# Kernel tuning notes

Hardware: AMD Instinct MI355X
Metric: run time of the kernel (lower is better)

Reference implementation:

```python
import jax, jax.numpy as jnp
import numpy as np
from jax import lax

OBS_LEN = 8
PRED_LEN = 12
DIM = 128      # hidden_dim
EMB = 64       # embedding_dim
HEADS = 4
MODES = 5
SCENE = 32     # peds per scene
NPED = 8192    # total peds (256 scenes)


def _lin(key, out_d, in_d):
    kw, kb = jax.random.split(key)
    w = jax.random.normal(kw, (out_d, in_d), jnp.float32) / np.sqrt(in_d).astype(np.float32)
    b = jax.random.normal(kb, (out_d,), jnp.float32) * 0.01
    return w, b


def _stack(key, n, out_d, in_d):
    ws, bs = zip(*[_lin(k, out_d, in_d) for k in jax.random.split(key, n)])
    return jnp.stack(ws), jnp.stack(bs)


def setup_inputs() -> dict:
    key = jax.random.key(0)
    ks = jax.random.split(key, 24)
    inp = {}
    inp['obs_traj'] = jax.random.normal(ks[0], (OBS_LEN, NPED, 2), jnp.float32)
    inp['pe_w'], inp['pe_b'] = _lin(ks[1], EMB, 2)
    inp['lstm_wih'], inp['lstm_bih'] = _lin(ks[2], 4 * DIM, EMB)
    inp['lstm_whh'], inp['lstm_bhh'] = _lin(ks[3], 4 * DIM, DIM)
    inp['rp_w1'], inp['rp_b1'] = _lin(ks[4], DIM // 2, 2)
    inp['rp_w2'], inp['rp_b2'] = _lin(ks[5], DIM, DIM // 2)
    inp['wq'], inp['bq'] = _lin(ks[6], DIM, DIM)
    inp['wk'], inp['bk'] = _lin(ks[7], DIM, DIM)
    inp['wv'], inp['bv'] = _lin(ks[8], DIM, DIM)
    inp['wo'], inp['bo'] = _lin(ks[9], DIM, DIM)
    inp['op_w'], inp['op_b'] = _lin(ks[10], DIM, 2 * DIM)
    inp['mp_w1'], inp['mp_b1'] = _lin(ks[11], DIM, 2 * DIM)
    inp['mp_w2'], inp['mp_b2'] = _lin(ks[12], MODES, DIM)
    inp['td_w1'], inp['td_b1'] = _stack(ks[13], MODES, DIM, 2 * DIM)
    inp['td_w2'], inp['td_b2'] = _stack(ks[14], MODES, DIM, DIM)
    inp['td_w3'], inp['td_b3'] = _stack(ks[15], MODES, PRED_LEN * 2, DIM)
    inp['ud_w1'], inp['ud_b1'] = _stack(ks[16], MODES, DIM // 2, 2 * DIM)
    inp['ud_w2'], inp['ud_b2'] = _stack(ks[17], MODES, PRED_LEN * 2, DIM // 2)
    inp['scene_size'] = SCENE
    return inp


def reference(obs_traj, pe_w, pe_b, lstm_wih, lstm_bih, lstm_whh, lstm_bhh,
              rp_w1, rp_b1, rp_w2, rp_b2, wq, bq, wk, bk, wv, bv, wo, bo,
              op_w, op_b, mp_w1, mp_b1, mp_w2, mp_b2,
              td_w1, td_b1, td_w2, td_b2, td_w3, td_b3,
              ud_w1, ud_b1, ud_w2, ud_b2, scene_size):
    obs = jnp.transpose(obs_traj, (1, 0, 2))          # (N, T, 2)
    N = obs.shape[0]
    D = lstm_whh.shape[1]

    # ---- NodeHistoryEncoder: Linear embed + 1-layer LSTM, last hidden ----
    emb = jnp.einsum('ntd,ed->nte', obs, pe_w) + pe_b  # (N, T, EMB)

    def step(carry, x):
        h, c = carry
        g = x @ lstm_wih.T + lstm_bih + h @ lstm_whh.T + lstm_bhh
        i, f, gg, o = jnp.split(g, 4, axis=-1)          # torch gate order i,f,g,o
        c = jax.nn.sigmoid(f) * c + jax.nn.sigmoid(i) * jnp.tanh(gg)
        h = jax.nn.sigmoid(o) * jnp.tanh(c)
        return (h, c), None

    h0 = jnp.zeros((N, D), obs.dtype)
    (node_features, _), _ = lax.scan(step, (h0, h0), jnp.swapaxes(emb, 0, 1))
    last_pos = obs[:, -1, :]                            # (N, 2)

    # ---- EdgeEncoder: per-scene rel-pos-biased multi-head attention ----
    S = scene_size
    B = N // S
    feat = node_features.reshape(B, S, D)
    pos = last_pos.reshape(B, S, 2)
    rel = pos[:, None, :, :] - pos[:, :, None, :]       # [b,i,j] = pos_j - pos_i
    rel_enc = jax.nn.relu(jnp.einsum('bijd,hd->bijh', rel, rp_w1) + rp_b1)
    rel_enc = jnp.einsum('bijh,eh->bije', rel_enc, rp_w2) + rp_b2  # (B,S,S,D)
    kv = feat[:, None, :, :] + rel_enc                  # key == value
    dh = D // HEADS
    q = (feat @ wq.T + bq).reshape(B, S, HEADS, dh)
    kp = (jnp.einsum('bijd,ed->bije', kv, wk) + bk).reshape(B, S, S, HEADS, dh)
    vp = (jnp.einsum('bijd,ed->bije', kv, wv) + bv).reshape(B, S, S, HEADS, dh)
    scores = jnp.einsum('bihd,bijhd->bhij', q, kp) / np.sqrt(dh).astype(np.float32)
    attn = jax.nn.softmax(scores, axis=-1)
    ctx = jnp.einsum('bhij,bijhd->bihd', attn, vp).reshape(B, S, D)
    attn_out = ctx @ wo.T + bo
    edge = (jnp.concatenate([feat, attn_out], axis=-1) @ op_w.T + op_b).reshape(N, D)

    f_all = jnp.concatenate([node_features, edge], axis=-1)  # (N, 2D)

    # ---- GMMDecoder ----
    probs = jax.nn.softmax(jax.nn.relu(f_all @ mp_w1.T + mp_b1) @ mp_w2.T + mp_b2, axis=-1)
    h1 = jax.nn.relu(jnp.einsum('nd,mhd->nmh', f_all, td_w1) + td_b1)    # (N,M,D)
    h2 = jax.nn.relu(jnp.einsum('nmh,mgh->nmg', h1, td_w2) + td_b2)
    traj = (jnp.einsum('nmg,mog->nmo', h2, td_w3) + td_b3).reshape(N, MODES, PRED_LEN, 2)
    u1 = jax.nn.relu(jnp.einsum('nd,mhd->nmh', f_all, ud_w1) + ud_b1)
    sigmas = jax.nn.softplus(jnp.einsum('nmh,moh->nmo', u1, ud_w2) + ud_b2).reshape(N, MODES, PRED_LEN, 2)
    predictions = jnp.cumsum(traj, axis=2) + last_pos[:, None, None, :]
    return predictions, probs
```

## Files before the change

### kernel.cpp

```cpp
#include <hip/hip_runtime.h>
#include <math.h>

typedef __attribute__((ext_vector_type(8))) short short8;
typedef __attribute__((ext_vector_type(4))) float f32x4;

#define NPED 8192
#define INVS 0.1767766952966369f

#define B_WHH    0
#define B_WQKV   131072
#define B_WK2PAD 294912
#define B_OPWE   360448
#define B_MPW1   425984
#define B_TDW1   491520
#define B_TDW2   819200
#define B_TDW3C  983040
#define F_WIHE   1024000
#define F_BEFF   1028096
#define F_WV2T   1030144
#define F_BQKV   1062912
#define F_BEDGE  1065472
#define F_TDB3C  1065984
#define A_FEAT   1066496
#define A_QKV    3163648

__device__ __forceinline__ float bf2f(ushort u) {
  union { unsigned i; float f; } v; v.i = ((unsigned)u) << 16; return v.f;
}
__device__ __forceinline__ float blo(unsigned u) {
  union { unsigned i; float f; } v; v.i = u << 16; return v.f;
}
__device__ __forceinline__ float bhi(unsigned u) {
  union { unsigned i; float f; } v; v.i = u & 0xffff0000u; return v.f;
}
__device__ __forceinline__ ushort f2bf(float f) {
  union { float f; unsigned i; } v; v.f = f;
  unsigned r = v.i + 0x7fffu + ((v.i >> 16) & 1u);
  return (ushort)(r >> 16);
}

__global__ __launch_bounds__(256) void prep(
    const float* __restrict__ wih, const float* __restrict__ bih, const float* __restrict__ bhh,
    const float* __restrict__ pew, const float* __restrict__ peb,
    const float* __restrict__ wk, const float* __restrict__ wv,
    const float* __restrict__ rpw2, const float* __restrict__ rpb2,
    const float* __restrict__ bq, const float* __restrict__ bk, const float* __restrict__ bv,
    const float* __restrict__ whh, const float* __restrict__ wq, const float* __restrict__ wo,
    const float* __restrict__ opw, const float* __restrict__ opb, const float* __restrict__ bo,
    const float* __restrict__ mpw1,
    const float* __restrict__ tdw1, const float* __restrict__ tdw2,
    const float* __restrict__ tdw3, const float* __restrict__ tdb3,
    char* __restrict__ wsb) {
  int tid = blockIdx.x * 256 + threadIdx.x;
  if (tid < 512) {
    int d = tid;
    float s0 = 0.f, s1 = 0.f, sb = 0.f;
    for (int e = 0; e < 64; ++e) {
      float w = wih[d * 64 + e];
      s0 += w * pew[e * 2]; s1 += w * pew[e * 2 + 1]; sb += w * peb[e];
    }
    ((float*)(wsb + F_WIHE))[d * 2] = s0;
    ((float*)(wsb + F_WIHE))[d * 2 + 1] = s1;
    ((float*)(wsb + F_BEFF))[d] = bih[d] + bhh[d] + sb;
  } else if (tid < 49664) {
    int j = tid - 512; int n = j >> 7, k = j & 127;
    float v = (n < 128) ? wq[n * 128 + k] * INVS
                        : (n < 256) ? wk[(n - 128) * 128 + k] : wv[(n - 256) * 128 + k];
    ((ushort*)(wsb + B_WQKV))[j] = f2bf(v);
  } else if (tid < 82432) {
    int idx = tid - 49664; int r = idx >> 7, d = idx & 127;
    int h = r >> 6, e = r & 63;
    float s = 0.f;
    if ((d >> 5) == h)
      for (int c = 0; c < 128; ++c) s += wk[d * 128 + c] * rpw2[c * 64 + e];
    ((ushort*)(wsb + B_WK2PAD))[idx] = f2bf(s);
  } else if (tid < 115200) {
    int idx = tid - 82432; int o = idx >> 8, k = idx & 255;
    float s;
    if (k < 128) s = opw[o * 256 + k];
    else {
      s = 0.f;
      for (int c = 0; c < 128; ++c) s += opw[o * 256 + 128 + c] * wo[c * 128 + (k - 128)];
    }
    ((ushort*)(wsb + B_OPWE))[idx] = f2bf(s);
  } else if (tid < 147968) {
    int j = tid - 115200; ((ushort*)(wsb + B_MPW1))[j] = f2bf(mpw1[j]);
  } else if (tid < 311808) {
    int j = tid - 147968; ((ushort*)(wsb + B_TDW1))[j] = f2bf(tdw1[j]);
  } else if (tid < 393728) {
    int j = tid - 311808; ((ushort*)(wsb + B_TDW2))[j] = f2bf(tdw2[j]);
  } else if (tid < 414208) {
    int j = tid - 393728; int m = j >> 12, r = j & 4095, o = r >> 7, k = r & 127;
    float s = 0.f;
    if (o < 24) {
      int c = o & 1, jj = o >> 1;
      for (int jp = 0; jp <= jj; ++jp) s += tdw3[(m * 24 + jp * 2 + c) * 128 + k];
    }
    ((ushort*)(wsb + B_TDW3C))[j] = f2bf(s);
  } else if (tid < 414328) {
    int j = tid - 414208; int m = j / 24, o = j % 24;
    int c = o & 1, jj = o >> 1;
    float s = 0.f;
    for (int jp = 0; jp <= jj; ++jp) s += tdb3[m * 24 + jp * 2 + c];
    ((float*)(wsb + F_TDB3C))[j] = s;
  } else if (tid < 414968) {
    int d = tid - 414328;
    float s = 0.f;
    if (d < 128) s = bq[d] * INVS;
    else if (d < 256) {
      int dd = d - 128; s = bk[dd];
      for (int c = 0; c < 128; ++c) s += wk[dd * 128 + c] * rpb2[c];
    } else if (d < 384) {
      int dd = d - 256; s = bv[dd];
      for (int c = 0; c < 128; ++c) s += wv[dd * 128 + c] * rpb2[c];
    }
    ((float*)(wsb + F_BQKV))[d] = s;
  } else if (tid < 415096) {
    int o = tid - 414968;
    float s = opb[o];
    for (int c = 0; c < 128; ++c) s += opw[o * 256 + 128 + c] * bo[c];
    ((float*)(wsb + F_BEDGE))[o] = s;
  } else if (tid < 423288) {
    int idx = tid - 415096; int e = idx >> 7, hd = idx & 127;
    float s = 0.f;
    for (int c = 0; c < 128; ++c) s += wv[hd * 128 + c] * rpw2[c * 64 + e];
    ((float*)(wsb + F_WV2T))[idx] = s;
  } else if (tid < 488824) {
    int i = tid - 423288;
    ((ushort*)(wsb + B_WHH))[i] = f2bf(whh[i]);
  }
}

__global__ __launch_bounds__(256) void prep2(
    const ushort* __restrict__ wk2pad, const float* __restrict__ wq,
    const float* __restrict__ bq, ushort* __restrict__ wqkv, float* __restrict__ bqkv) {
  int idx = blockIdx.x * 256 + threadIdx.x;
  if (idx < 32768) {
    int e = idx >> 7, k = idx & 127, h = e >> 6;
    float s = 0.f;
    for (int dd = 0; dd < 32; ++dd) {
      int d = h * 32 + dd;
      s += bf2f(wk2pad[e * 128 + d]) * wq[d * 128 + k];
    }
    wqkv[(384 + e) * 128 + k] = f2bf(s * INVS);
  } else if (idx < 33024) {
    int e = idx - 32768, h = e >> 6;
    float s = 0.f;
    for (int dd = 0; dd < 32; ++dd) {
      int d = h * 32 + dd;
      s += bf2f(wk2pad[e * 128 + d]) * bq[d];
    }
    bqkv[384 + e] = s * INVS;
  }
}

__global__ __launch_bounds__(512) void lstm_mfma(
    const float* __restrict__ obs, const ushort* __restrict__ whhb,
    const float* __restrict__ wihe, const float* __restrict__ beff,
    ushort* __restrict__ feat) {
  __shared__ ushort Hs[32 * 128];
  __shared__ float obs_s[8][32][2];
  int tid = threadIdx.x;
  int w = tid >> 6, l = tid & 63;
  int lm = l & 15, lg = l >> 4;
  int nb = blockIdx.x * 32;
  {
    int ts = tid >> 6, p = (tid >> 1) & 31, c = tid & 1;
    obs_s[ts][p][c] = obs[ts * (NPED * 2) + (nb + p) * 2 + c];
  }
  for (int i = tid; i < 4096; i += 512) Hs[i] = 0;
  short8 bfr[4][4];
  float wx0[4], wx1[4], be[4];
#pragma unroll
  for (int q = 0; q < 4; ++q) {
    int g = q * 128 + w * 16 + lm;
    wx0[q] = wihe[g * 2]; wx1[q] = wihe[g * 2 + 1]; be[q] = beff[g];
#pragma unroll
    for (int ks = 0; ks < 4; ++ks)
      bfr[q][ks] = *(const short8*)(const void*)&whhb[g * 128 + ks * 32 + lg * 8];
  }
  float cst[2][4] = {};
  __syncthreads();
  for (int ts = 0; ts < 8; ++ts) {
    f32x4 acc[2][4];
#pragma unroll
    for (int mi = 0; mi < 2; ++mi)
#pragma unroll
      for (int r = 0; r < 4; ++r) {
        int p = mi * 16 + lg * 4 + r;
        float ox = obs_s[ts][p][0], oy = obs_s[ts][p][1];
#pragma unroll
        for (int q = 0; q < 4; ++q)
          acc[mi][q][r] = be[q] + wx0[q] * ox + wx1[q] * oy;
      }
#pragma unroll
    for (int ks = 0; ks < 4; ++ks) {
      int p0 = lm, p1 = 16 + lm;
      short8 a0 = *(const short8*)(const void*)&Hs[p0 * 128 + ((ks * 32 + lg * 8) ^ ((p0 & 7) << 3))];
      short8 a1 = *(const short8*)(const void*)&Hs[p1 * 128 + ((ks * 32 + lg * 8) ^ ((p1 & 7) << 3))];
#pragma unroll
      for (int q = 0; q < 4; ++q) {
        acc[0][q] = __builtin_amdgcn_mfma_f32_16x16x32_bf16(a0, bfr[q][ks], acc[0][q], 0, 0, 0);
        acc[1][q] = __builtin_amdgcn_mfma_f32_16x16x32_bf16(a1, bfr[q][ks], acc[1][q], 0, 0, 0);
      }
    }
    __syncthreads();
    int d = w * 16 + lm;
#pragma unroll
    for (int mi = 0; mi < 2; ++mi)
#pragma unroll
      for (int r = 0; r < 4; ++r) {
        int p = mi * 16 + lg * 4 + r;
        float xi = acc[mi][0][r], xf = acc[mi][1][r], xg = acc[mi][2][r], xo = acc[mi][3][r];
        float ig = 1.f / (1.f + __expf(-xi));
        float fg = 1.f / (1.f + __expf(-xf));
        xg = fminf(fmaxf(xg, -30.f), 30.f);
        float eg = __expf(-2.f * xg);
        float gg = (1.f - eg) / (1.f + eg);
        float og = 1.f / (1.f + __expf(-xo));
        float cv = fg * cst[mi][r] + ig * gg;
        cst[mi][r] = cv;
        float cvc = fminf(fmaxf(cv, -30.f), 30.f);
        float ec = __expf(-2.f * cvc);
        float th = (1.f - ec) / (1.f + ec);
        ushort hb = f2bf(og * th);
        Hs[p * 128 + (d ^ ((p & 7) << 3))] = hb;
        if (ts == 7) feat[(size_t)(nb + p) * 128 + d] = hb;
      }
    __syncthreads();
  }
}

template<int NF, int NKS, int K1KS, int RS>
__global__ __launch_bounds__(256) void mfma_gemm(
    const ushort* __restrict__ A1, int lda1,
    const ushort* __restrict__ A2, int lda2,
    const ushort* __restrict__ Bw,
    const float* __restrict__ bias,
    ushort* __restrict__ out, int ldo, int ooff, int relu) {
  int w = threadIdx.x >> 6, l = threadIdx.x & 63;
  int lm = l & 15, lg = l >> 4;
  int row, col0, orow0;
  if (RS) {
    row = blockIdx.x * 32 + (w >> 1) * 16 + lm;
    col0 = blockIdx.y * (NF * 32) + (w & 1) * (NF * 16);
    orow0 = blockIdx.x * 32 + (w >> 1) * 16 + lg * 4;
  } else {
    row = blockIdx.x * 64 + w * 16 + lm;
    col0 = blockIdx.y * (NF * 16);
    orow0 = blockIdx.x * 64 + w * 16 + lg * 4;
  }
  f32x4 acc[NF];
#pragma unroll
  for (int i = 0; i < NF; ++i) acc[i] = (f32x4){0.f, 0.f, 0.f, 0.f};
#pragma unroll
  for (int ks = 0; ks < NKS; ++ks) {
    int kb = ks * 32 + lg * 8;
    const ushort* ap = (ks < K1KS) ? (A1 + (size_t)row * lda1 + kb)
                                   : (A2 + (size_t)row * lda2 + (kb - K1KS * 32));
    short8 af = *(const short8*)(const void*)ap;
#pragma unroll
    for (int ni = 0; ni < NF; ++ni) {
      short8 bf = *(const short8*)(const void*)(Bw + (size_t)(col0 + ni * 16 + lm) * (NKS * 32) + kb);
      acc[ni] = __builtin_amdgcn_mfma_f32_16x16x32_bf16(af, bf, acc[ni], 0, 0, 0);
    }
  }
#pragma unroll
  for (int ni = 0; ni < NF; ++ni) {
    int c = col0 + ni * 16 + lm;
    float bv = bias[c];
#pragma unroll
    for (int r = 0; r < 4; ++r) {
      float v = acc[ni][r] + bv;
      if (relu) v = fmaxf(v, 0.f);
      out[(size_t)(orow0 + r) * ldo + ooff + c] = f2bf(v);
    }
  }
}

__global__ __launch_bounds__(256) void td_mp(
    const ushort* __restrict__ feat, const ushort* __restrict__ qkv,
    const ushort* __restrict__ w1b, const float* __restrict__ tdb1,
    const ushort* __restrict__ w2b, const float* __restrict__ tdb2,
    const ushort* __restrict__ w3c, const float* __restrict__ b3c,
    const float* __restrict__ mpw1b, const float* __restrict__ mpb1,
    const float* __restrict__ mpw2, const float* __restrict__ mpb2,
    const float* __restrict__ obs, float* __restrict__ out) {
  __shared__ float smem[32 * 72];
  int t = threadIdx.x, w = t >> 6, l = t & 63, lm = l & 15, lg = l >> 4;
  int wr = w >> 1, wc = w & 1;
  int z = blockIdx.y;

  if (z < 5) {
    ushort* slab = (ushort*)smem;
    int m = z;
    int row = blockIdx.x * 32 + wr * 16 + lm;
    const ushort* W1 = w1b + (size_t)m * 32768;
    const ushort* W2 = w2b + (size_t)m * 16384;
    const ushort* W3 = w3c + (size_t)m * 4096;
    const float* B1 = tdb1 + m * 128;
    const float* B2 = tdb2 + m * 128;
    f32x4 a1[4];
#pragma unroll
    for (int i = 0; i < 4; ++i) a1[i] = (f32x4){0.f, 0.f, 0.f, 0.f};
#pragma unroll
    for (int ks = 0; ks < 8; ++ks) {
      int kb = ks * 32 + lg * 8;
      const ushort* ap = (ks < 4) ? (feat + (size_t)row * 128 + kb)
                                  : (qkv + (size_t)row * 640 + 256 + (kb - 128));
      short8 af = *(const short8*)(const void*)ap;
#pragma unroll
      for (int ni = 0; ni < 4; ++ni) {
        short8 bf = *(const short8*)(const void*)(W1 + (size_t)(wc * 64 + ni * 16 + lm) * 256 + kb);
        a1[ni] = __builtin_amdgcn_mfma_f32_16x16x32_bf16(af, bf, a1[ni], 0, 0, 0);
      }
    }
#pragma unroll
    for (int ni = 0; ni < 4; ++ni) {
      int c = wc * 64 + ni * 16 + lm;
      float bb = B1[c];
#pragma unroll
      for (int r = 0; r < 4; ++r)
        slab[(wr * 16 + lg * 4 + r) * 136 + c] = f2bf(fmaxf(a1[ni][r] + bb, 0.f));
    }
    __syncthreads();
    short8 af2[4];
#pragma unroll
    for (int ks = 0; ks < 4; ++ks)
      af2[ks] = *(const short8*)(const void*)&slab[(wr * 16 + lm) * 136 + ks * 32 + lg * 8];
    f32x4 a2[4];
#pragma unroll
    for (int i = 0; i < 4; ++i) a2[i] = (f32x4){0.f, 0.f, 0.f, 0.f};
#pragma unroll
    for (int ks = 0; ks < 4; ++ks) {
      int kb = ks * 32 + lg * 8;
#pragma unroll
      for (int ni = 0; ni < 4; ++ni) {
        short8 bf = *(const short8*)(const void*)(W2 + (size_t)(wc * 64 + ni * 16 + lm) * 128 + kb);
        a2[ni] = __builtin_amdgcn_mfma_f32_16x16x32_bf16(af2[ks], bf, a2[ni], 0, 0, 0);
      }
    }
    __syncthreads();
#pragma unroll
    for (int ni = 0; ni < 4; ++ni) {
      int c = wc * 64 + ni * 16 + lm;
      float bb = B2[c];
#pragma unroll
      for (int r = 0; r < 4; ++r)
        slab[(wr * 16 + lg * 4 + r) * 136 + c] = f2bf(fmaxf(a2[ni][r] + bb, 0.f));
    }
    __syncthreads();
    short8 af3[4], w3f[4];
#pragma unroll
    for (int ks = 0; ks < 4; ++ks) {
      af3[ks] = *(const short8*)(const void*)&slab[(wr * 16 + lm) * 136 + ks * 32 + lg * 8];
      w3f[ks] = *(const short8*)(const void*)(W3 + (size_t)(wc * 16 + lm) * 128 + ks * 32 + lg * 8);
    }
    f32x4 a3 = (f32x4){0.f, 0.f, 0.f, 0.f};
#pragma unroll
    for (int ks = 0; ks < 4; ++ks)
      a3 = __builtin_amdgcn_mfma_f32_16x16x32_bf16(af3[ks], w3f[ks], a3, 0, 0, 0);
    int o = wc * 16 + lm;
    if (o < 24) {
      float bb = b3c[m * 24 + o];
      int c = o & 1;
#pragma unroll
      for (int r = 0; r < 4; ++r) {
        int n = blockIdx.x * 32 + wr * 16 + lg * 4 + r;
        out[(size_t)n * 120 + m * 24 + o] = a3[r] + bb + obs[7 * (NPED * 2) + n * 2 + c];
      }
    }
  } else {
    float* w2s = smem;
    float* pc  = smem + 640;
    for (int i = t; i < 640; i += 256) w2s[(i >> 7) * 128 + (i & 127)] = mpw2[i];
    int g = wr, ch = wc, cb = ch * 64;
    int row = blockIdx.x * 32 + g * 16 + lm;
    f32x4 acc[4];
#pragma unroll
    for (int i = 0; i < 4; ++i) acc[i] = (f32x4){0.f, 0.f, 0.f, 0.f};
#pragma unroll
    for (int ks = 0; ks < 8; ++ks) {
      int kb = ks * 32 + lg * 8;
      const ushort* ap = (ks < 4) ? (feat + (size_t)row * 128 + kb)
                                  : (qkv + (size_t)row * 640 + 256 + (kb - 128));
      short8 af = *(const short8*)(const void*)ap;
#pragma unroll
      for (int ni = 0; ni < 4; ++ni) {
        short8 bf = *(const short8*)(const void*)((const ushort*)mpw1b + (size_t)(cb + ni * 16 + lm) * 256 + kb);
        acc[ni] = __builtin_amdgcn_mfma_f32_16x16x32_bf16(af, bf, acc[ni], 0, 0, 0);
      }
    }
    __syncthreads();
    float bc[4];
#pragma unroll
    for (int ni = 0; ni < 4; ++ni) bc[ni] = mpb1[cb + ni * 16 + lm];
    float lgt[4][5];
#pragma unroll
    for (int r = 0; r < 4; ++r)
#pragma unroll
      for (int m = 0; m < 5; ++m) {
        float s = 0.f;
#pragma unroll
        for (int ni = 0; ni < 4; ++ni)
          s += fmaxf(acc[ni][r] + bc[ni], 0.f) * w2s[m * 128 + cb + ni * 16 + lm];
        lgt[r][m] = s;
      }
#pragma unroll
    for (int mask = 1; mask < 16; mask <<= 1)
#pragma unroll
      for (int r = 0; r < 4; ++r)
#pragma unroll
        for (int m = 0; m < 5; ++m)
          lgt[r][m] += __shfl_xor(lgt[r][m], mask);
    if (ch == 1 && lm < 5) {
#pragma unroll
      for (int r = 0; r < 4; ++r) pc[(g * 16 + lg * 4 + r) * 5 + lm] = lgt[r][lm];
    }
    __syncthreads();
    if (ch == 0 && lm < 5) {
#pragma unroll
      for (int r = 0; r < 4; ++r) {
        float lv[5], mx = -1e30f, sm = 0.f;
#pragma unroll
        for (int m = 0; m < 5; ++m) {
          lv[m] = lgt[r][m] + pc[(g * 16 + lg * 4 + r) * 5 + m] + mpb2[m];
          mx = fmaxf(mx, lv[m]);
        }
#pragma unroll
        for (int m = 0; m < 5; ++m) { lv[m] = expf(lv[m] - mx); sm += lv[m]; }
        int n = blockIdx.x * 32 + g * 16 + lg * 4 + r;
        out[983040 + (size_t)n * 5 + lm] = lv[lm] / sm;
      }
    }
  }
}

__global__ __launch_bounds__(256) void attn_kernel(
    const float* __restrict__ obs, ushort* QKV,
    const float* __restrict__ wv2T,
    const float* __restrict__ rpw1, const float* __restrict__ rpb1) {
  __shared__ ushort K0s[32 * 128];
  __shared__ ushort V0s[32 * 128];
  __shared__ ushort renc[4 * 32 * 64];
  __shared__ float Qi[4][128];
  __shared__ float QWs[4][256];
  __shared__ float att[4][4][32];
  __shared__ float AR[4][4][64];
  __shared__ float rpx[64], rpy[64], rpb[64];
  __shared__ float posS[32][2];
  __shared__ float posI[4][2];
  int t = threadIdx.x;
  int scene = blockIdx.x & 255, ic = blockIdx.x >> 8;
  int i0 = ic * 4, sbase = scene * 32;

  for (int idx = t; idx < 1024; idx += 256) {
    int arr = idx >> 9, j = (idx >> 4) & 31, c = idx & 15;
    short8 v = *(const short8*)(const void*)&QKV[(size_t)(sbase + j) * 640 + 128 + arr * 128 + c * 8];
    ushort* dst = arr ? V0s : K0s;
    *(short8*)(void*)&dst[j * 128 + (c ^ (j & 7)) * 8] = v;
  }
  for (int idx = t; idx < 512; idx += 256) {
    int ii = idx >> 7, d = idx & 127;
    Qi[ii][d] = bf2f(QKV[(size_t)(sbase + i0 + ii) * 640 + d]);
  }
  for (int idx = t; idx < 1024; idx += 256) {
    int ii = idx >> 8, e = idx & 255;
    QWs[ii][e] = bf2f(QKV[(size_t)(sbase + i0 + ii) * 640 + 384 + e]);
  }
  if (t < 64) posS[t >> 1][t & 1] = obs[7 * (NPED * 2) + (sbase + (t >> 1)) * 2 + (t & 1)];
  else if (t < 72) {
    int q = t - 64;
    posI[q >> 1][q & 1] = obs[7 * (NPED * 2) + (sbase + i0 + (q >> 1)) * 2 + (q & 1)];
  } else if (t >= 128 && t < 192) {
    int e = t - 128;
    rpx[e] = rpw1[e * 2]; rpy[e] = rpw1[e * 2 + 1]; rpb[e] = rpb1[e];
  }
  __syncthreads();

  for (int idx = t; idx < 1024; idx += 256) {
    int ii = idx >> 8, j = (idx >> 3) & 31, c = idx & 7;
    float dx = posS[j][0] - posI[ii][0], dy = posS[j][1] - posI[ii][1];
    short8 pk;
#pragma unroll
    for (int r = 0; r < 8; ++r) {
      int e = c * 8 + r;
      pk[r] = (short)f2bf(fmaxf(rpx[e] * dx + rpy[e] * dy + rpb[e], 0.f));
    }
    *(short8*)(void*)&renc[(ii * 32 + j) * 64 + (c ^ (j & 7)) * 8] = pk;
  }
  __syncthreads();

  for (int idx = t; idx < 512; idx += 256) {
    int ii = idx >> 7, h = (idx >> 5) & 3, j = idx & 31;
    float s = 0.f;
#pragma unroll
    for (int cc = 0; cc < 4; ++cc) {
      uint4 kv = *(const uint4*)(const void*)&K0s[j * 128 + (((h * 4 + cc) ^ (j & 7)) * 8)];
      const float4 qa = *(const float4*)&Qi[ii][h * 32 + cc * 8];
      const float4 qb = *(const float4*)&Qi[ii][h * 32 + cc * 8 + 4];
      s += blo(kv.x) * qa.x + bhi(kv.x) * qa.y + blo(kv.y) * qa.z + bhi(kv.y) * qa.w;
      s += blo(kv.z) * qb.x + bhi(kv.z) * qb.y + blo(kv.w) * qb.z + bhi(kv.w) * qb.w;
    }
#pragma unroll
    for (int c = 0; c < 8; ++c) {
      uint4 rv = *(const uint4*)(const void*)&renc[(ii * 32 + j) * 64 + ((c ^ (j & 7)) * 8)];
      const float4 ua = *(const float4*)&QWs[ii][h * 64 + c * 8];
      const float4 ub = *(const float4*)&QWs[ii][h * 64 + c * 8 + 4];
      s += blo(rv.x) * ua.x + bhi(rv.x) * ua.y + blo(rv.y) * ua.z + bhi(rv.y) * ua.w;
      s += blo(rv.z) * ub.x + bhi(rv.z) * ub.y + blo(rv.w) * ub.z + bhi(rv.w) * ub.w;
    }
    att[ii][h][j] = s;
  }
  __syncthreads();

  {
    int r = t >> 4, lj = t & 15;
    float v0 = att[r >> 2][r & 3][lj], v1 = att[r >> 2][r & 3][lj + 16];
    float mx = fmaxf(v0, v1);
    mx = fmaxf(mx, __shfl_xor(mx, 8, 16));
    mx = fmaxf(mx, __shfl_xor(mx, 4, 16));
    mx = fmaxf(mx, __shfl_xor(mx, 2, 16));
    mx = fmaxf(mx, __shfl_xor(mx, 1, 16));
    float e0 = expf(v0 - mx), e1 = expf(v1 - mx);
    float sm = e0 + e1;
    sm += __shfl_xor(sm, 8, 16);
    sm += __shfl_xor(sm, 4, 16);
    sm += __shfl_xor(sm, 2, 16);
    sm += __shfl_xor(sm, 1, 16);
    float inv = 1.f / sm;
    att[r >> 2][r & 3][lj] = e0 * inv;
    att[r >> 2][r & 3][lj + 16] = e1 * inv;
  }
  __syncthreads();

  {
    int ii = t >> 6, h = (t >> 4) & 3, e4 = t & 15;
    int c = e4 >> 1, off = (e4 & 1) * 4;
    float a0 = 0.f, a1 = 0.f, a2 = 0.f, a3 = 0.f;
    for (int j = 0; j < 32; ++j) {
      float av = att[ii][h][j];
      uint2 rv = *(const uint2*)(const void*)&renc[(ii * 32 + j) * 64 + ((c ^ (j & 7)) * 8) + off];
      a0 += av * blo(rv.x); a1 += av * bhi(rv.x);
      a2 += av * blo(rv.y); a3 += av * bhi(rv.y);
    }
    *(float4*)&AR[ii][h][e4 * 4] = make_float4(a0, a1, a2, a3);
  }
  __syncthreads();

  {
    int ii = t >> 6, l = t & 63;
    int h5 = l >> 5, hd4 = l & 31;
    int hd = hd4 * 4, h = hd >> 5;
    float c0 = 0.f, c1 = 0.f, c2 = 0.f, c3 = 0.f;
    int cch = hd >> 3, offh = hd & 7;
    for (int j = h5 * 16; j < h5 * 16 + 16; ++j) {
      float av = att[ii][h][j];
      uint2 vv = *(const uint2*)(const void*)&V0s[j * 128 + ((cch ^ (j & 7)) * 8) + offh];
      c0 += av * blo(vv.x); c1 += av * bhi(vv.x);
      c2 += av * blo(vv.y); c3 += av * bhi(vv.y);
    }
    for (int e4 = h5 * 8; e4 < h5 * 8 + 8; ++e4) {
      const float4 ar = *(const float4*)&AR[ii][h][e4 * 4];
#pragma unroll
      for (int r = 0; r < 4; ++r) {
        const float4 wv = *(const float4*)&wv2T[(e4 * 4 + r) * 128 + hd];
        float a = (r == 0) ? ar.x : (r == 1) ? ar.y : (r == 2) ? ar.z : ar.w;
        c0 += a * wv.x; c1 += a * wv.y; c2 += a * wv.z; c3 += a * wv.w;
      }
    }
    c0 += __shfl_xor(c0, 32); c1 += __shfl_xor(c1, 32);
    c2 += __shfl_xor(c2, 32); c3 += __shfl_xor(c3, 32);
    if (h5 == 0) {
      ushort4 o;
      o.x = f2bf(c0); o.y = f2bf(c1); o.z = f2bf(c2); o.w = f2bf(c3);
      *(ushort4*)(void*)&QKV[(size_t)(sbase + i0 + ii) * 640 + hd] = o;
    }
  }
}

extern "C" void kernel_launch(void* const* d_in, const int* in_sizes, int n_in,
                              void* d_out, int out_size, void* d_ws, size_t ws_size,
                              hipStream_t stream) {
  (void)in_sizes; (void)n_in; (void)out_size; (void)ws_size;
  const float* obs  = (const float*)d_in[0];
  const float* pew  = (const float*)d_in[1];
  const float* peb  = (const float*)d_in[2];
  const float* wih  = (const float*)d_in[3];
  const float* bih  = (const float*)d_in[4];
  const float* whh  = (const float*)d_in[5];
  const float* bhh  = (const float*)d_in[6];
  const float* rpw1 = (const float*)d_in[7];
  const float* rpb1 = (const float*)d_in[8];
  const float* rpw2 = (const float*)d_in[9];
  const float* rpb2 = (const float*)d_in[10];
  const float* wq   = (const float*)d_in[11];
  const float* bq   = (const float*)d_in[12];
  const float* wk   = (const float*)d_in[13];
  const float* bk   = (const float*)d_in[14];
  const float* wv   = (const float*)d_in[15];
  const float* bv   = (const float*)d_in[16];
  const float* wo   = (const float*)d_in[17];
  const float* bo   = (const float*)d_in[18];
  const float* opw  = (const float*)d_in[19];
  const float* opb  = (const float*)d_in[20];
  const float* mpw1 = (const float*)d_in[21];
  const float* mpb1 = (const float*)d_in[22];
  const float* mpw2 = (const float*)d_in[23];
  const float* mpb2 = (const float*)d_in[24];
  const float* tdw1 = (const float*)d_in[25];
  const float* tdb1 = (const float*)d_in[26];
  const float* tdw2 = (const float*)d_in[27];
  const float* tdb2 = (const float*)d_in[28];
  const float* tdw3 = (const float*)d_in[29];
  const float* tdb3 = (const float*)d_in[30];
  char* wsb = (char*)d_ws;
  float* out = (float*)d_out;

  ushort* whhb   = (ushort*)(wsb + B_WHH);
  ushort* wqkvb  = (ushort*)(wsb + B_WQKV);
  ushort* wk2pb  = (ushort*)(wsb + B_WK2PAD);
  ushort* opweb  = (ushort*)(wsb + B_OPWE);
  ushort* mpw1b  = (ushort*)(wsb + B_MPW1);
  ushort* tdw1b  = (ushort*)(wsb + B_TDW1);
  ushort* tdw2b  = (ushort*)(wsb + B_TDW2);
  ushort* tdw3cb = (ushort*)(wsb + B_TDW3C);
  ushort* featb  = (ushort*)(wsb + A_FEAT);
  ushort* qkvb   = (ushort*)(wsb + A_QKV);

  prep<<<1910, 256, 0, stream>>>(wih, bih, bhh, pew, peb, wk, wv, rpw2, rpb2,
                                 bq, bk, bv, whh, wq, wo, opw, opb, bo, mpw1,
                                 tdw1, tdw2, tdw3, tdb3, wsb);
  prep2<<<129, 256, 0, stream>>>(wk2pb, wq, bq, wqkvb, (float*)(wsb + F_BQKV));
  lstm_mfma<<<256, 512, 0, stream>>>(obs, whhb, (float*)(wsb + F_WIHE),
                                     (float*)(wsb + F_BEFF), featb);
  mfma_gemm<4, 4, 4, 0><<<dim3(128, 10), 256, 0, stream>>>(
      featb, 128, featb, 128, wqkvb, (float*)(wsb + F_BQKV), qkvb, 640, 0, 0);
  attn_kernel<<<2048, 256, 0, stream>>>(obs, qkvb, (float*)(wsb + F_WV2T), rpw1, rpb1);
  mfma_gemm<2, 8, 4, 1><<<dim3(256, 2), 256, 0, stream>>>(
      featb, 128, qkvb, 640, opweb, (float*)(wsb + F_BEDGE), qkvb, 640, 256, 0);
  td_mp<<<dim3(256, 6), 256, 0, stream>>>(featb, qkvb, tdw1b, tdb1, tdw2b, tdb2,
                                          tdw3cb, (float*)(wsb + F_TDB3C),
                                          (const float*)mpw1b, mpb1, mpw2, mpb2, obs, out);
}
```

Before: 265.5 us.

## Fuse QKV GEMM into LSTM, edge GEMM into decoder, merge prep kernels

The QKV projection now runs at the tail of the LSTM kernel, reading the final hidden state straight from shared memory. The edge projection is recomputed inside each decoder block (six times per row tile) and kept in shared memory. prep2 is folded into prep by recomputing the wk·rpw2 product inline. This removes three kernel launches and the global round trips for feat-to-qkv and edge. In exchange it adds redundant edge GEMM work per z-slice and a heavier serial inner loop in prep.

```diff
diff --git a/kernel.cpp b/kernel.cpp
--- a/kernel.cpp
+++ b/kernel.cpp
@@ -9,20 +9,19 @@
 
 #define B_WHH    0
 #define B_WQKV   131072
-#define B_WK2PAD 294912
-#define B_OPWE   360448
-#define B_MPW1   425984
-#define B_TDW1   491520
-#define B_TDW2   819200
-#define B_TDW3C  983040
-#define F_WIHE   1024000
-#define F_BEFF   1028096
-#define F_WV2T   1030144
-#define F_BQKV   1062912
-#define F_BEDGE  1065472
-#define F_TDB3C  1065984
-#define A_FEAT   1066496
-#define A_QKV    3163648
+#define B_OPWE   294912
+#define B_MPW1   360448
+#define B_TDW1   425984
+#define B_TDW2   753664
+#define B_TDW3C  917504
+#define F_WIHE   958464
+#define F_BEFF   962560
+#define F_WV2T   964608
+#define F_BQKV   997376
+#define F_BEDGE  999936
+#define F_TDB3C  1000448
+#define A_FEAT   1001472
+#define A_QKV    3098624
 
 __device__ __forceinline__ float bf2f(ushort u) {
   union { unsigned i; float f; } v; v.i = ((unsigned)u) << 16; return v.f;
@@ -68,14 +67,7 @@
                         : (n < 256) ? wk[(n - 128) * 128 + k] : wv[(n - 256) * 128 + k];
     ((ushort*)(wsb + B_WQKV))[j] = f2bf(v);
   } else if (tid < 82432) {
-    int idx = tid - 49664; int r = idx >> 7, d = idx & 127;
-    int h = r >> 6, e = r & 63;
-    float s = 0.f;
-    if ((d >> 5) == h)
-      for (int c = 0; c < 128; ++c) s += wk[d * 128 + c] * rpw2[c * 64 + e];
-    ((ushort*)(wsb + B_WK2PAD))[idx] = f2bf(s);
-  } else if (tid < 115200) {
-    int idx = tid - 82432; int o = idx >> 8, k = idx & 255;
+    int idx = tid - 49664; int o = idx >> 8, k = idx & 255;
     float s;
     if (k < 128) s = opw[o * 256 + k];
     else {
@@ -83,81 +75,80 @@
       for (int c = 0; c < 128; ++c) s += opw[o * 256 + 128 + c] * wo[c * 128 + (k - 128)];
     }
     ((ushort*)(wsb + B_OPWE))[idx] = f2bf(s);
-  } else if (tid < 147968) {
-    int j = tid - 115200; ((ushort*)(wsb + B_MPW1))[j] = f2bf(mpw1[j]);
-  } else if (tid < 311808) {
-    int j = tid - 147968; ((ushort*)(wsb + B_TDW1))[j] = f2bf(tdw1[j]);
-  } else if (tid < 393728) {
-    int j = tid - 311808; ((ushort*)(wsb + B_TDW2))[j] = f2bf(tdw2[j]);
-  } else if (tid < 414208) {
-    int j = tid - 393728; int m = j >> 12, r = j & 4095, o = r >> 7, k = r & 127;
+  } else if (tid < 115200) {
+    int j = tid - 82432; ((ushort*)(wsb + B_MPW1))[j] = f2bf(mpw1[j]);
+  } else if (tid < 279040) {
+    int j = tid - 115200; ((ushort*)(wsb + B_TDW1))[j] = f2bf(tdw1[j]);
+  } else if (tid < 360960) {
+    int j = tid - 279040; ((ushort*)(wsb + B_TDW2))[j] = f2bf(tdw2[j]);
+  } else if (tid < 381440) {
+    int j = tid - 360960; int m = j >> 12, r = j & 4095, o = r >> 7, k = r & 127;
     float s = 0.f;
     if (o < 24) {
       int c = o & 1, jj = o >> 1;
       for (int jp = 0; jp <= jj; ++jp) s += tdw3[(m * 24 + jp * 2 + c) * 128 + k];
     }
     ((ushort*)(wsb + B_TDW3C))[j] = f2bf(s);
-  } else if (tid < 414328) {
-    int j = tid - 414208; int m = j / 24, o = j % 24;
+  } else if (tid < 381560) {
+    int j = tid - 381440; int m = j / 24, o = j % 24;
     int c = o & 1, jj = o >> 1;
     float s = 0.f;
     for (int jp = 0; jp <= jj; ++jp) s += tdb3[m * 24 + jp * 2 + c];
     ((float*)(wsb + F_TDB3C))[j] = s;
-  } else if (tid < 414968) {
-    int d = tid - 414328;
-    float s = 0.f;
+  } else if (tid < 381944) {
+    int d = tid - 381560;
+    float s;
     if (d < 128) s = bq[d] * INVS;
     else if (d < 256) {
       int dd = d - 128; s = bk[dd];
       for (int c = 0; c < 128; ++c) s += wk[dd * 128 + c] * rpb2[c];
-    } else if (d < 384) {
+    } else {
       int dd = d - 256; s = bv[dd];
       for (int c = 0; c < 128; ++c) s += wv[dd * 128 + c] * rpb2[c];
     }
     ((float*)(wsb + F_BQKV))[d] = s;
-  } else if (tid < 415096) {
-    int o = tid - 414968;
+  } else if (tid < 382072) {
+    int o = tid - 381944;
     float s = opb[o];
     for (int c = 0; c < 128; ++c) s += opw[o * 256 + 128 + c] * bo[c];
     ((float*)(wsb + F_BEDGE))[o] = s;
-  } else if (tid < 423288) {
-    int idx = tid - 415096; int e = idx >> 7, hd = idx & 127;
+  } else if (tid < 390264) {
+    int idx = tid - 382072; int e = idx >> 7, hd = idx & 127;
     float s = 0.f;
     for (int c = 0; c < 128; ++c) s += wv[hd * 128 + c] * rpw2[c * 64 + e];
     ((float*)(wsb + F_WV2T))[idx] = s;
-  } else if (tid < 488824) {
-    int i = tid - 423288;
+  } else if (tid < 455800) {
+    int i = tid - 390264;
     ((ushort*)(wsb + B_WHH))[i] = f2bf(whh[i]);
-  }
-}
-
-__global__ __launch_bounds__(256) void prep2(
-    const ushort* __restrict__ wk2pad, const float* __restrict__ wq,
-    const float* __restrict__ bq, ushort* __restrict__ wqkv, float* __restrict__ bqkv) {
-  int idx = blockIdx.x * 256 + threadIdx.x;
-  if (idx < 32768) {
-    int e = idx >> 7, k = idx & 127, h = e >> 6;
+  } else if (tid < 488568) {
+    int idx = tid - 455800; int e = idx >> 7, k = idx & 127;
+    int h = e >> 6, e6 = e & 63;
     float s = 0.f;
     for (int dd = 0; dd < 32; ++dd) {
       int d = h * 32 + dd;
-      s += bf2f(wk2pad[e * 128 + d]) * wq[d * 128 + k];
-    }
-    wqkv[(384 + e) * 128 + k] = f2bf(s * INVS);
-  } else if (idx < 33024) {
-    int e = idx - 32768, h = e >> 6;
+      float wk2ed = 0.f;
+      for (int c = 0; c < 128; ++c) wk2ed += wk[d * 128 + c] * rpw2[c * 64 + e6];
+      s += wk2ed * wq[d * 128 + k];
+    }
+    ((ushort*)(wsb + B_WQKV))[(384 + e) * 128 + k] = f2bf(s * INVS);
+  } else if (tid < 488824) {
+    int e = tid - 488568; int h = e >> 6, e6 = e & 63;
     float s = 0.f;
     for (int dd = 0; dd < 32; ++dd) {
       int d = h * 32 + dd;
-      s += bf2f(wk2pad[e * 128 + d]) * bq[d];
-    }
-    bqkv[384 + e] = s * INVS;
-  }
-}
-
-__global__ __launch_bounds__(512) void lstm_mfma(
+      float wk2ed = 0.f;
+      for (int c = 0; c < 128; ++c) wk2ed += wk[d * 128 + c] * rpw2[c * 64 + e6];
+      s += wk2ed * bq[d];
+    }
+    ((float*)(wsb + F_BQKV))[384 + e] = s * INVS;
+  }
+}
+
+__global__ __launch_bounds__(512) void lstm_qkv(
     const float* __restrict__ obs, const ushort* __restrict__ whhb,
     const float* __restrict__ wihe, const float* __restrict__ beff,
-    ushort* __restrict__ feat) {
+    const ushort* __restrict__ wqkv, const float* __restrict__ bqkv,
+    ushort* __restrict__ feat, ushort* __restrict__ qkvb) {
   __shared__ ushort Hs[32 * 128];
   __shared__ float obs_s[8][32][2];
   int tid = threadIdx.x;
@@ -229,72 +220,83 @@
       }
     __syncthreads();
   }
-}
-
-template<int NF, int NKS, int K1KS, int RS>
-__global__ __launch_bounds__(256) void mfma_gemm(
-    const ushort* __restrict__ A1, int lda1,
-    const ushort* __restrict__ A2, int lda2,
-    const ushort* __restrict__ Bw,
-    const float* __restrict__ bias,
-    ushort* __restrict__ out, int ldo, int ooff, int relu) {
-  int w = threadIdx.x >> 6, l = threadIdx.x & 63;
-  int lm = l & 15, lg = l >> 4;
-  int row, col0, orow0;
-  if (RS) {
-    row = blockIdx.x * 32 + (w >> 1) * 16 + lm;
-    col0 = blockIdx.y * (NF * 32) + (w & 1) * (NF * 16);
-    orow0 = blockIdx.x * 32 + (w >> 1) * 16 + lg * 4;
-  } else {
-    row = blockIdx.x * 64 + w * 16 + lm;
-    col0 = blockIdx.y * (NF * 16);
-    orow0 = blockIdx.x * 64 + w * 16 + lg * 4;
-  }
-  f32x4 acc[NF];
-#pragma unroll
-  for (int i = 0; i < NF; ++i) acc[i] = (f32x4){0.f, 0.f, 0.f, 0.f};
-#pragma unroll
-  for (int ks = 0; ks < NKS; ++ks) {
+  int wr2 = w >> 2, wc2 = w & 3;
+  f32x4 qacc[10];
+#pragma unroll
+  for (int i = 0; i < 10; ++i) qacc[i] = (f32x4){0.f, 0.f, 0.f, 0.f};
+#pragma unroll
+  for (int ks = 0; ks < 4; ++ks) {
+    int p = wr2 * 16 + lm;
+    short8 af = *(const short8*)(const void*)&Hs[p * 128 + ((ks * 32 + lg * 8) ^ ((p & 7) << 3))];
     int kb = ks * 32 + lg * 8;
-    const ushort* ap = (ks < K1KS) ? (A1 + (size_t)row * lda1 + kb)
-                                   : (A2 + (size_t)row * lda2 + (kb - K1KS * 32));
-    short8 af = *(const short8*)(const void*)ap;
-#pragma unroll
-    for (int ni = 0; ni < NF; ++ni) {
-      short8 bf = *(const short8*)(const void*)(Bw + (size_t)(col0 + ni * 16 + lm) * (NKS * 32) + kb);
-      acc[ni] = __builtin_amdgcn_mfma_f32_16x16x32_bf16(af, bf, acc[ni], 0, 0, 0);
-    }
-  }
-#pragma unroll
-  for (int ni = 0; ni < NF; ++ni) {
-    int c = col0 + ni * 16 + lm;
-    float bv = bias[c];
+#pragma unroll
+    for (int ni = 0; ni < 10; ++ni) {
+      int col = wc2 * 160 + ni * 16 + lm;
+      short8 bf = *(const short8*)(const void*)&wqkv[(size_t)col * 128 + kb];
+      qacc[ni] = __builtin_amdgcn_mfma_f32_16x16x32_bf16(af, bf, qacc[ni], 0, 0, 0);
+    }
+  }
+#pragma unroll
+  for (int ni = 0; ni < 10; ++ni) {
+    int col = wc2 * 160 + ni * 16 + lm;
+    float bv = bqkv[col];
 #pragma unroll
     for (int r = 0; r < 4; ++r) {
-      float v = acc[ni][r] + bv;
-      if (relu) v = fmaxf(v, 0.f);
-      out[(size_t)(orow0 + r) * ldo + ooff + c] = f2bf(v);
+      int row = nb + wr2 * 16 + lg * 4 + r;
+      qkvb[(size_t)row * 640 + col] = f2bf(qacc[ni][r] + bv);
     }
   }
 }
 
 __global__ __launch_bounds__(256) void td_mp(
     const ushort* __restrict__ feat, const ushort* __restrict__ qkv,
+    const ushort* __restrict__ opwe, const float* __restrict__ bedge,
     const ushort* __restrict__ w1b, const float* __restrict__ tdb1,
     const ushort* __restrict__ w2b, const float* __restrict__ tdb2,
     const ushort* __restrict__ w3c, const float* __restrict__ b3c,
-    const float* __restrict__ mpw1b, const float* __restrict__ mpb1,
+    const ushort* __restrict__ mpw1b, const float* __restrict__ mpb1,
     const float* __restrict__ mpw2, const float* __restrict__ mpb2,
     const float* __restrict__ obs, float* __restrict__ out) {
-  __shared__ float smem[32 * 72];
+  __shared__ __align__(16) char smem_raw[8576 * 2];
+  ushort* edge_s = (ushort*)smem_raw;
+  ushort* slab   = (ushort*)(smem_raw + 8576);
+  float*  w2s    = (float*)(smem_raw + 8576);
+  float*  pc     = (float*)(smem_raw + 8576 + 2560);
   int t = threadIdx.x, w = t >> 6, l = t & 63, lm = l & 15, lg = l >> 4;
   int wr = w >> 1, wc = w & 1;
   int z = blockIdx.y;
+  int row = blockIdx.x * 32 + wr * 16 + lm;
+
+  {
+    f32x4 ea[4];
+#pragma unroll
+    for (int i = 0; i < 4; ++i) ea[i] = (f32x4){0.f, 0.f, 0.f, 0.f};
+#pragma unroll
+    for (int ks = 0; ks < 8; ++ks) {
+      int kb = ks * 32 + lg * 8;
+      const ushort* ap = (ks < 4) ? (feat + (size_t)row * 128 + kb)
+                                  : (qkv + (size_t)row * 640 + (kb - 128));
+      short8 af = *(const short8*)(const void*)ap;
+#pragma unroll
+      for (int ni = 0; ni < 4; ++ni) {
+        int c = wc * 64 + ni * 16 + lm;
+        short8 bf = *(const short8*)(const void*)(opwe + (size_t)c * 256 + kb);
+        ea[ni] = __builtin_amdgcn_mfma_f32_16x16x32_bf16(af, bf, ea[ni], 0, 0, 0);
+      }
+    }
+#pragma unroll
+    for (int ni = 0; ni < 4; ++ni) {
+      int c = wc * 64 + ni * 16 + lm;
+      float bb = bedge[c];
+#pragma unroll
+      for (int r = 0; r < 4; ++r)
+        edge_s[(wr * 16 + lg * 4 + r) * 134 + c] = f2bf(ea[ni][r] + bb);
+    }
+  }
+  __syncthreads();
 
   if (z < 5) {
-    ushort* slab = (ushort*)smem;
     int m = z;
-    int row = blockIdx.x * 32 + wr * 16 + lm;
     const ushort* W1 = w1b + (size_t)m * 32768;
     const ushort* W2 = w2b + (size_t)m * 16384;
     const ushort* W3 = w3c + (size_t)m * 4096;
@@ -306,9 +308,9 @@
 #pragma unroll
     for (int ks = 0; ks < 8; ++ks) {
       int kb = ks * 32 + lg * 8;
-      const ushort* ap = (ks < 4) ? (feat + (size_t)row * 128 + kb)
-                                  : (qkv + (size_t)row * 640 + 256 + (kb - 128));
-      short8 af = *(const short8*)(const void*)ap;
+      short8 af;
+      if (ks < 4) af = *(const short8*)(const void*)(feat + (size_t)row * 128 + kb);
+      else        af = *(const short8*)(const void*)&edge_s[(wr * 16 + lm) * 134 + (kb - 128)];
 #pragma unroll
       for (int ni = 0; ni < 4; ++ni) {
         short8 bf = *(const short8*)(const void*)(W1 + (size_t)(wc * 64 + ni * 16 + lm) * 256 + kb);
@@ -321,13 +323,13 @@
       float bb = B1[c];
 #pragma unroll
       for (int r = 0; r < 4; ++r)
-        slab[(wr * 16 + lg * 4 + r) * 136 + c] = f2bf(fmaxf(a1[ni][r] + bb, 0.f));
+        slab[(wr * 16 + lg * 4 + r) * 134 + c] = f2bf(fmaxf(a1[ni][r] + bb, 0.f));
     }
     __syncthreads();
     short8 af2[4];
 #pragma unroll
     for (int ks = 0; ks < 4; ++ks)
-      af2[ks] = *(const short8*)(const void*)&slab[(wr * 16 + lm) * 136 + ks * 32 + lg * 8];
+      af2[ks] = *(const short8*)(const void*)&slab[(wr * 16 + lm) * 134 + ks * 32 + lg * 8];
     f32x4 a2[4];
 #pragma unroll
     for (int i = 0; i < 4; ++i) a2[i] = (f32x4){0.f, 0.f, 0.f, 0.f};
@@ -347,13 +349,13 @@
       float bb = B2[c];
 #pragma unroll
       for (int r = 0; r < 4; ++r)
-        slab[(wr * 16 + lg * 4 + r) * 136 + c] = f2bf(fmaxf(a2[ni][r] + bb, 0.f));
+        slab[(wr * 16 + lg * 4 + r) * 134 + c] = f2bf(fmaxf(a2[ni][r] + bb, 0.f));
     }
     __syncthreads();
     short8 af3[4], w3f[4];
 #pragma unroll
     for (int ks = 0; ks < 4; ++ks) {
-      af3[ks] = *(const short8*)(const void*)&slab[(wr * 16 + lm) * 136 + ks * 32 + lg * 8];
+      af3[ks] = *(const short8*)(const void*)&slab[(wr * 16 + lm) * 134 + ks * 32 + lg * 8];
       w3f[ks] = *(const short8*)(const void*)(W3 + (size_t)(wc * 16 + lm) * 128 + ks * 32 + lg * 8);
     }
     f32x4 a3 = (f32x4){0.f, 0.f, 0.f, 0.f};
@@ -371,23 +373,20 @@
       }
     }
   } else {
-    float* w2s = smem;
-    float* pc  = smem + 640;
-    for (int i = t; i < 640; i += 256) w2s[(i >> 7) * 128 + (i & 127)] = mpw2[i];
+    for (int i = t; i < 640; i += 256) w2s[i] = mpw2[i];
     int g = wr, ch = wc, cb = ch * 64;
-    int row = blockIdx.x * 32 + g * 16 + lm;
     f32x4 acc[4];
 #pragma unroll
     for (int i = 0; i < 4; ++i) acc[i] = (f32x4){0.f, 0.f, 0.f, 0.f};
 #pragma unroll
     for (int ks = 0; ks < 8; ++ks) {
       int kb = ks * 32 + lg * 8;
-      const ushort* ap = (ks < 4) ? (feat + (size_t)row * 128 + kb)
-                                  : (qkv + (size_t)row * 640 + 256 + (kb - 128));
-      short8 af = *(const short8*)(const void*)ap;
+      short8 af;
+      if (ks < 4) af = *(const short8*)(const void*)(feat + (size_t)row * 128 + kb);
+      else        af = *(const short8*)(const void*)&edge_s[(wr * 16 + lm) * 134 + (kb - 128)];
 #pragma unroll
       for (int ni = 0; ni < 4; ++ni) {
-        short8 bf = *(const short8*)(const void*)((const ushort*)mpw1b + (size_t)(cb + ni * 16 + lm) * 256 + kb);
+        short8 bf = *(const short8*)(const void*)(mpw1b + (size_t)(cb + ni * 16 + lm) * 256 + kb);
         acc[ni] = __builtin_amdgcn_mfma_f32_16x16x32_bf16(af, bf, acc[ni], 0, 0, 0);
       }
     }
@@ -619,7 +618,6 @@
 
   ushort* whhb   = (ushort*)(wsb + B_WHH);
   ushort* wqkvb  = (ushort*)(wsb + B_WQKV);
-  ushort* wk2pb  = (ushort*)(wsb + B_WK2PAD);
   ushort* opweb  = (ushort*)(wsb + B_OPWE);
   ushort* mpw1b  = (ushort*)(wsb + B_MPW1);
   ushort* tdw1b  = (ushort*)(wsb + B_TDW1);
@@ -631,15 +629,12 @@
   prep<<<1910, 256, 0, stream>>>(wih, bih, bhh, pew, peb, wk, wv, rpw2, rpb2,
                                  bq, bk, bv, whh, wq, wo, opw, opb, bo, mpw1,
                                  tdw1, tdw2, tdw3, tdb3, wsb);
-  prep2<<<129, 256, 0, stream>>>(wk2pb, wq, bq, wqkvb, (float*)(wsb + F_BQKV));
-  lstm_mfma<<<256, 512, 0, stream>>>(obs, whhb, (float*)(wsb + F_WIHE),
-                                     (float*)(wsb + F_BEFF), featb);
-  mfma_gemm<4, 4, 4, 0><<<dim3(128, 10), 256, 0, stream>>>(
-      featb, 128, featb, 128, wqkvb, (float*)(wsb + F_BQKV), qkvb, 640, 0, 0);
+  lstm_qkv<<<256, 512, 0, stream>>>(obs, whhb, (float*)(wsb + F_WIHE),
+                                    (float*)(wsb + F_BEFF), wqkvb,
+                                    (float*)(wsb + F_BQKV), featb, qkvb);
   attn_kernel<<<2048, 256, 0, stream>>>(obs, qkvb, (float*)(wsb + F_WV2T), rpw1, rpb1);
-  mfma_gemm<2, 8, 4, 1><<<dim3(256, 2), 256, 0, stream>>>(
-      featb, 128, qkvb, 640, opweb, (float*)(wsb + F_BEDGE), qkvb, 640, 256, 0);
-  td_mp<<<dim3(256, 6), 256, 0, stream>>>(featb, qkvb, tdw1b, tdb1, tdw2b, tdb2,
+  td_mp<<<dim3(256, 6), 256, 0, stream>>>(featb, qkvb, opweb, (float*)(wsb + F_BEDGE),
+                                          tdw1b, tdb1, tdw2b, tdb2,
                                           tdw3cb, (float*)(wsb + F_TDB3C),
-                                          (const float*)mpw1b, mpb1, mpw2, mpb2, obs, out);
-}
+                                          mpw1b, mpb1, mpw2, mpb2, obs, out);
+}
```

Measured after the change: 410.0 us. +54.4%, slower.
